# Optimization experiments

Measured on AMD Instinct MI355X. Metric: run time of the kernel, lower is better.

Reference implementation:

```python
import jax, jax.numpy as jnp
import numpy as np

NUM_CLASSES = 81
THRESHOLD = 0.5
NEGPOS_RATIO = 3
VAR = (0.1, 0.2)


def setup_inputs() -> dict:
    key = jax.random.key(0)
    kl, kc, kp1, kp2, kt1, kt2, klab = jax.random.split(key, 7)
    B, P, T = 64, 8732, 16
    loc_data = jax.random.normal(kl, (B, P, 4), jnp.float32)
    conf_data = jax.random.normal(kc, (B, P, NUM_CLASSES), jnp.float32)
    # priors in center-form (cx, cy, w, h), w/h strictly positive
    cxcy = jax.random.uniform(kp1, (P, 2), jnp.float32)
    wh = 0.05 + 0.45 * jax.random.uniform(kp2, (P, 2), jnp.float32)
    priors = jnp.concatenate([cxcy, wh], axis=1)
    # ground-truth boxes in point-form (xmin, ymin, xmax, ymax), valid in [0,1]
    mins = 0.7 * jax.random.uniform(kt1, (B, T, 2), jnp.float32)
    sizes = 0.05 + 0.25 * jax.random.uniform(kt2, (B, T, 2), jnp.float32)
    truth_boxes = jnp.concatenate([mins, mins + sizes], axis=-1)
    labels = jax.random.randint(klab, (B, T), 0, NUM_CLASSES - 1, jnp.int32)
    return {"loc_data": loc_data, "conf_data": conf_data, "priors": priors,
            "truth_boxes": truth_boxes, "labels": labels}


def _point_form(pr):
    # center-form -> point-form
    return jnp.concatenate([pr[:, :2] - pr[:, 2:] / 2, pr[:, :2] + pr[:, 2:] / 2], axis=1)


def _intersect(box_a, box_b):
    # [T,4] x [P,4] -> [T,P] intersection areas (the repo uses raw intersection, not IoU)
    max_xy = jnp.minimum(box_a[:, None, 2:], box_b[None, :, 2:])
    min_xy = jnp.maximum(box_a[:, None, :2], box_b[None, :, :2])
    inter = jnp.clip(max_xy - min_xy, 0.0, None)
    return inter[..., 0] * inter[..., 1]


def _encode(matched, priors):
    g_cxcy = (matched[:, :2] + matched[:, 2:4]) / 2 - priors[:, :2]
    g_cxcy = g_cxcy / (VAR[0] * priors[:, 2:])
    g_wh = (matched[:, 2:4] - matched[:, :2]) / priors[:, 2:]
    g_wh = jnp.log(g_wh + 1e-10) / VAR[1]
    return jnp.concatenate([g_cxcy, g_wh], axis=1)


def _match(truths, labels, priors):
    # truths [T,4] point-form, labels [T], priors [P,4] center-form
    T = truths.shape[0]
    P = priors.shape[0]
    overlaps = _intersect(truths, _point_form(priors))          # [T,P]
    best_prior_idx = jnp.argmax(overlaps, axis=1)               # [T]
    best_truth_overlap = jnp.max(overlaps, axis=0)              # [P]
    best_truth_idx = jnp.argmax(overlaps, axis=0)               # [P]
    # ensure each gt's best prior is kept (overlap forced to 2)
    best_truth_overlap = best_truth_overlap.at[best_prior_idx].set(2.0)
    hit = best_prior_idx[:, None] == jnp.arange(P)[None, :]     # [T,P]
    last_j = jnp.max(jnp.where(hit, jnp.arange(T)[:, None], -1), axis=0)  # [P]
    best_truth_idx = jnp.where(last_j >= 0, last_j, best_truth_idx)
    matches = truths[best_truth_idx]                            # [P,4]
    conf = jnp.where(best_truth_overlap < THRESHOLD, 0,
                     labels[best_truth_idx] + 1).astype(jnp.int32)
    return _encode(matches, priors), conf


def _smooth_l1(d):
    ad = jnp.abs(d)
    return jnp.where(ad < 1.0, 0.5 * d * d, ad - 0.5)


def _forward(loc_data, conf_data, priors, truth_boxes, labels):
    B, P, C = conf_data.shape
    loc_t, conf_t = jax.vmap(_match, in_axes=(0, 0, None))(truth_boxes, labels, priors)
    pos = conf_t > 0                                            # [B,P]
    num_pos = pos.sum(axis=1, keepdims=True)                    # [B,1]
    # localization smooth-L1 over positives (sum reduction)
    loss_l = jnp.sum(jnp.where(pos[..., None], _smooth_l1(loc_data - loc_t), 0.0))
    # per-prior cross-entropy
    logp = jax.nn.log_softmax(conf_data, axis=-1)               # [B,P,C]
    ce = -jnp.take_along_axis(logp, conf_t[..., None], axis=-1)[..., 0]  # [B,P]
    # hard-negative mining via double argsort rank
    mined = jnp.where(pos, 0.0, ce)
    order = jnp.argsort(-mined, axis=1)
    rank = jnp.argsort(order, axis=1)
    num_neg = jnp.clip(NEGPOS_RATIO * num_pos, None, P - 1)     # [B,1]
    neg = rank < num_neg
    loss_c = jnp.sum(jnp.where(pos | neg, ce, 0.0))
    N = jnp.maximum(num_pos.sum(), 1).astype(loc_data.dtype)
    return loss_l / N, loss_c / N


def reference(loc_data, conf_data, priors, truth_boxes, labels):
    return _forward(loc_data, conf_data, priors, truth_boxes, labels)
```

## Files before the change

kernel.cpp:

```cpp
#include <hip/hip_runtime.h>
#include <float.h>
#include <math.h>

#define B_NUM 64
#define P_NUM 8732
#define T_NUM 16
#define C_NUM 81
#define TPB   512
#define RPB_LSE 128
#define NBLK_LSE ((B_NUM * P_NUM) / RPB_LSE)
#define GRID1 (B_NUM + NBLK_LSE)
#define PLMAX 32

__device__ __forceinline__ float smooth_l1(float d) {
    float ad = fabsf(d);
    return (ad < 1.0f) ? 0.5f * d * d : ad - 0.5f;
}

struct MatchSh {
    float s_t[T_NUM][4];
    int   s_lab[T_NUM];
    unsigned short s_m[P_NUM];
    float s_rv[8 * T_NUM];
    int   s_ri[8 * T_NUM];
    int   s_bp[T_NUM];
    float s_red[8];
    int   s_redi[8];
    int   s_plist[PLMAX];
    int   s_pcount;
};

__global__ __launch_bounds__(TPB, 4) void k_fused1(
    const float* __restrict__ loc, const float* __restrict__ conf,
    const float* __restrict__ priors, const float* __restrict__ truths,
    const int* __restrict__ labels,
    int* __restrict__ num_pos, float* __restrict__ loss_l_b,
    float* __restrict__ negce, int* __restrict__ plist_g,
    int* __restrict__ sel_ctr)
{
    __shared__ MatchSh shm;
    const int tid = threadIdx.x;
    const int lane = tid & 63, wv = tid >> 6;

    if (blockIdx.x >= B_NUM) {
        const int r0 = (blockIdx.x - B_NUM) * RPB_LSE;
        const int g  = lane >> 4;
        const int lg = lane & 15;
        const int gr0 = r0 + wv * 16 + g * 4;
        const float4* g4 = (const float4*)(conf) + (size_t)gr0 * 81 / 4;

        float4 q0 = g4[lg];
        float4 q1 = g4[lg + 16];
        float4 q2 = g4[lg + 32];
        float4 q3 = g4[lg + 48];
        float4 q4 = g4[lg + 64];
        float4 q5 = make_float4(0.f, 0.f, 0.f, 0.f);
        if (lg == 0) q5 = g4[80];

        float x0 = 0.0f;
        if (lg == 0)  x0 = q0.x;
        if (lg == 4)  x0 = q1.y;
        if (lg == 8)  x0 = q2.z;
        if (lg == 12) x0 = q3.w;

        float a0 = 0.f, a1 = 0.f, a2 = 0.f, a3 = 0.f;
        a0 += __expf(q0.x) + __expf(q0.y) + __expf(q0.z) + __expf(q0.w);
        {
            int p = 64 + 4 * lg; float e;
            e = __expf(q1.x); if (p + 0 >= 81) a1 += e; else a0 += e;
            e = __expf(q1.y); if (p + 1 >= 81) a1 += e; else a0 += e;
            e = __expf(q1.z); if (p + 2 >= 81) a1 += e; else a0 += e;
            e = __expf(q1.w); if (p + 3 >= 81) a1 += e; else a0 += e;
        }
        {
            int p = 128 + 4 * lg; float e;
            e = __expf(q2.x); if (p + 0 >= 162) a2 += e; else a1 += e;
            e = __expf(q2.y); if (p + 1 >= 162) a2 += e; else a1 += e;
            e = __expf(q2.z); if (p + 2 >= 162) a2 += e; else a1 += e;
            e = __expf(q2.w); if (p + 3 >= 162) a2 += e; else a1 += e;
        }
        {
            int p = 192 + 4 * lg; float e;
            e = __expf(q3.x); if (p + 0 >= 243) a3 += e; else a2 += e;
            e = __expf(q3.y); if (p + 1 >= 243) a3 += e; else a2 += e;
            e = __expf(q3.z); if (p + 2 >= 243) a3 += e; else a2 += e;
            e = __expf(q3.w); if (p + 3 >= 243) a3 += e; else a2 += e;
        }
        a3 += __expf(q4.x) + __expf(q4.y) + __expf(q4.z) + __expf(q4.w);
        if (lg == 0)
            a3 += __expf(q5.x) + __expf(q5.y) + __expf(q5.z) + __expf(q5.w);

#pragma unroll
        for (int m = 1; m < 16; m <<= 1) {
            a0 += __shfl_xor(a0, m);
            a1 += __shfl_xor(a1, m);
            a2 += __shfl_xor(a2, m);
            a3 += __shfl_xor(a3, m);
        }
        if ((lg & 3) == 0) {
            int sel = lg >> 2;
            float s = (sel == 0) ? a0 : (sel == 1) ? a1 : (sel == 2) ? a2 : a3;
            negce[gr0 + sel] = __logf(s) - x0;
        }
        return;
    }

    const int b = blockIdx.x;
    if (tid == 0) {
        shm.s_pcount = 0;
        if (b == 0) *sel_ctr = 0;
    }
    if (tid < T_NUM * 4) ((float*)shm.s_t)[tid] = truths[b * T_NUM * 4 + tid];
    if (tid < T_NUM)     shm.s_lab[tid] = labels[b * T_NUM + tid];
    __syncthreads();

    float bpv[T_NUM]; int bpi[T_NUM];
#pragma unroll
    for (int t = 0; t < T_NUM; ++t) { bpv[t] = -1.0f; bpi[t] = 0; }

    const float4* pr4 = (const float4*)priors;
    for (int p = tid; p < P_NUM; p += TPB) {
        float4 pr = pr4[p];
        float px0 = pr.x - 0.5f * pr.z, py0 = pr.y - 0.5f * pr.w;
        float px1 = pr.x + 0.5f * pr.z, py1 = pr.y + 0.5f * pr.w;
        float btv = -1.0f; int bti = 0;
#pragma unroll
        for (int t = 0; t < T_NUM; ++t) {
            float ix = fminf(shm.s_t[t][2], px1) - fmaxf(shm.s_t[t][0], px0);
            float iy = fminf(shm.s_t[t][3], py1) - fmaxf(shm.s_t[t][1], py0);
            ix = fmaxf(ix, 0.0f); iy = fmaxf(iy, 0.0f);
            float ov = ix * iy;
            if (ov > btv) { btv = ov; bti = t; }
            if (ov > bpv[t]) { bpv[t] = ov; bpi[t] = p; }
        }
        shm.s_m[p] = (unsigned short)((btv >= 0.5f ? 0x8000 : 0) | bti);
    }
    __syncthreads();

#pragma unroll
    for (int t = 0; t < T_NUM; ++t) {
        float v = bpv[t]; int i = bpi[t];
#pragma unroll
        for (int off = 32; off > 0; off >>= 1) {
            float ov = __shfl_down(v, off);
            int   oi = __shfl_down(i, off);
            if (ov > v || (ov == v && oi < i)) { v = ov; i = oi; }
        }
        if (lane == 0) { shm.s_rv[wv * T_NUM + t] = v; shm.s_ri[wv * T_NUM + t] = i; }
    }
    __syncthreads();
    if (tid < T_NUM) {
        float v = shm.s_rv[tid]; int i = shm.s_ri[tid];
        for (int w = 1; w < 8; ++w) {
            float ov = shm.s_rv[w * T_NUM + tid]; int oi = shm.s_ri[w * T_NUM + tid];
            if (ov > v || (ov == v && oi < i)) { v = ov; i = oi; }
        }
        shm.s_bp[tid] = i;
    }
    __syncthreads();
    if (tid == 0) {
        for (int t = 0; t < T_NUM; ++t)
            shm.s_m[shm.s_bp[t]] = (unsigned short)(0x8000 | t);
    }
    __syncthreads();

    int cnt = 0; float lsum = 0.0f;
    const float4* loc4 = (const float4*)loc;
    for (int p = tid; p < P_NUM; p += TPB) {
        unsigned short mm = shm.s_m[p];
        if (mm & 0x8000) {
            int ti = mm & 0x7FFF;
            int c = shm.s_lab[ti] + 1;
            cnt++;
            int sl = atomicAdd(&shm.s_pcount, 1);
            if (sl < PLMAX) shm.s_plist[sl] = (p << 8) | c;
            float4 pr = pr4[p];
            float mx0 = shm.s_t[ti][0], my0 = shm.s_t[ti][1];
            float mx1 = shm.s_t[ti][2], my1 = shm.s_t[ti][3];
            float gx = ((mx0 + mx1) * 0.5f - pr.x) / (0.1f * pr.z);
            float gy = ((my0 + my1) * 0.5f - pr.y) / (0.1f * pr.w);
            float gw = __logf((mx1 - mx0) / pr.z + 1e-10f) / 0.2f;
            float gh = __logf((my1 - my0) / pr.w + 1e-10f) / 0.2f;
            float4 l = loc4[(size_t)b * P_NUM + p];
            lsum += smooth_l1(l.x - gx) + smooth_l1(l.y - gy)
                  + smooth_l1(l.z - gw) + smooth_l1(l.w - gh);
        }
    }
#pragma unroll
    for (int off = 32; off > 0; off >>= 1) {
        lsum += __shfl_down(lsum, off);
        cnt  += __shfl_down(cnt, off);
    }
    if (lane == 0) { shm.s_red[wv] = lsum; shm.s_redi[wv] = cnt; }
    __syncthreads();
    if (tid == 0) {
        float L = 0.0f; int C2 = 0;
        for (int w = 0; w < 8; ++w) { L += shm.s_red[w]; C2 += shm.s_redi[w]; }
        num_pos[b] = C2;
        loss_l_b[b] = L;
    }
    if (tid < shm.s_pcount && tid < PLMAX)
        plist_g[b * PLMAX + tid] = shm.s_plist[tid];
}

#define NQ4 2183
#define VELEMS 12

__global__ __launch_bounds__(1024) void k_select(
    const float* __restrict__ negce, const float* __restrict__ conf,
    const int* __restrict__ plist_g, const int* __restrict__ num_pos,
    float* __restrict__ loss_l_b, float* __restrict__ negsum_b,
    float* __restrict__ pce_b, int* __restrict__ sel_ctr,
    float* __restrict__ out)
{
    __shared__ int   s_wh[16][256];
    __shared__ int   s_hist[256];
    __shared__ unsigned int s_bm[273];
    __shared__ int   s_sel, s_rem;
    __shared__ float s_sv[16];
    __shared__ int   s_sc[16];
    __shared__ float s_pv[16];
    __shared__ int   s_last;
    __shared__ unsigned int s_mn[16], s_mx[16];
    __shared__ int   s_nz[16];
    __shared__ int   s_p1skip, s_p1sel, s_p1rem;

    const int b = blockIdx.x, tid = threadIdx.x;
    const int lane = tid & 63, wv = tid >> 6;

    const int np = num_pos[b];
    if (tid < 273) s_bm[tid] = 0u;
    __syncthreads();
    float pce = 0.0f;
    if (tid < np && tid < PLMAX) {
        int e = plist_g[b * PLMAX + tid];
        int p = e >> 8, c = e & 255;
        size_t idx = (size_t)b * P_NUM + p;
        size_t ci = idx * C_NUM;
        pce = negce[idx] + conf[ci] - conf[ci + c];
        atomicOr(&s_bm[p >> 5], 1u << (p & 31));
    }
    __syncthreads();

    unsigned int val[VELEMS];
    const float4* nb4 = (const float4*)(negce + (size_t)b * P_NUM);
#pragma unroll
    for (int i = 0; i < 3; ++i) {
        int q = tid + i * 1024;
        float4 v4 = make_float4(0.f, 0.f, 0.f, 0.f);
        if (q < NQ4) v4 = nb4[q];
        float vv[4] = {v4.x, v4.y, v4.z, v4.w};
#pragma unroll
        for (int k = 0; k < 4; ++k) {
            int p = 4 * q + k;
            unsigned int u = 0u;
            if (q < NQ4 && !((s_bm[p >> 5] >> (p & 31)) & 1u))
                u = __float_as_uint(fmaxf(vv[k], 0.0f));
            val[i * 4 + k] = u;
        }
    }

    int nn = 3 * np; if (nn > P_NUM - 1) nn = P_NUM - 1;

    {
        unsigned int tmn = 255u, tmx = 0u; int nz = 0;
#pragma unroll
        for (int i = 0; i < VELEMS; ++i) {
            unsigned int v = val[i];
            if (v) {
                unsigned int t = v >> 24;
                tmn = (t < tmn) ? t : tmn;
                tmx = (t > tmx) ? t : tmx;
                nz++;
            }
        }
#pragma unroll
        for (int off = 32; off > 0; off >>= 1) {
            unsigned int omn = __shfl_down(tmn, off);
            unsigned int omx = __shfl_down(tmx, off);
            int onz = __shfl_down(nz, off);
            tmn = (omn < tmn) ? omn : tmn;
            tmx = (omx > tmx) ? omx : tmx;
            nz += onz;
        }
        if (lane == 0) { s_mn[wv] = tmn; s_mx[wv] = tmx; s_nz[wv] = nz; }
        __syncthreads();
        if (tid == 0) {
            unsigned int MN = 255u, MX = 0u; int NZ = 0;
#pragma unroll
            for (int w = 0; w < 16; ++w) {
                if (s_mn[w] < MN) MN = s_mn[w];
                if (s_mx[w] > MX) MX = s_mx[w];
                NZ += s_nz[w];
            }
            int k0 = nn;
            if (MN == MX && NZ > 0) {
                s_p1skip = 1;
                if (k0 <= NZ) { s_p1sel = (int)MX; s_p1rem = k0; }
                else          { s_p1sel = 0;       s_p1rem = k0 - NZ; }
            } else {
                s_p1skip = 0;
            }
        }
        __syncthreads();
    }

    if (nn > 0) {
        unsigned int prefix = 0;
        int k = nn;
        const int shifts[4] = {24, 16, 8, 0};
        for (int si = 0; si < 4; ++si) {
            const int shift = shifts[si];
            if (si == 0 && s_p1skip) {
                prefix = ((unsigned int)s_p1sel) << 24;
                k = s_p1rem;
                continue;
            }
            for (int i = tid; i < 16 * 256; i += 1024) ((int*)s_wh)[i] = 0;
            __syncthreads();
            const unsigned int pmask = (shift == 24) ? 0u : (0xFFFFFFFFu << (shift + 8));
#pragma unroll
            for (int i = 0; i < VELEMS; ++i) {
                unsigned int v = val[i];
                if ((v & pmask) == prefix)
                    atomicAdd(&s_wh[wv][(v >> shift) & 0xFF], 1);
            }
            __syncthreads();
            if (tid < 256) {
                int s = 0;
#pragma unroll
                for (int w = 0; w < 16; ++w) s += s_wh[w][tid];
                s_hist[tid] = s;
            }
            __syncthreads();
            if (wv == 0) {
                int c0 = s_hist[4 * lane + 0], c1 = s_hist[4 * lane + 1];
                int c2 = s_hist[4 * lane + 2], c3 = s_hist[4 * lane + 3];
                int t3 = c3, t2 = c2 + t3, t1 = c1 + t2, t0 = c0 + t1;
                int g = t0, G = g;
#pragma unroll
                for (int off = 1; off < 64; off <<= 1) {
                    int o = __shfl_down(G, off);
                    if (lane + off < 64) G += o;
                }
                int above = G - g;
                int suf0 = t0 + above, suf1 = t1 + above;
                int suf2 = t2 + above, suf3 = t3 + above, suf4 = above;
                if (suf0 >= k && suf1 < k) { s_sel = 4 * lane + 0; s_rem = k - suf1; }
                if (suf1 >= k && suf2 < k) { s_sel = 4 * lane + 1; s_rem = k - suf2; }
                if (suf2 >= k && suf3 < k) { s_sel = 4 * lane + 2; s_rem = k - suf3; }
                if (suf3 >= k && suf4 < k) { s_sel = 4 * lane + 3; s_rem = k - suf4; }
            }
            __syncthreads();
            prefix |= ((unsigned int)s_sel) << shift;
            k = s_rem;
        }

        float sgt = 0.0f; int cgt = 0;
#pragma unroll
        for (int i = 0; i < VELEMS; ++i) {
            unsigned int v = val[i];
            if (v > prefix) { sgt += __uint_as_float(v); cgt++; }
        }
#pragma unroll
        for (int off = 32; off > 0; off >>= 1) {
            sgt += __shfl_down(sgt, off);
            cgt += __shfl_down(cgt, off);
        }
        if (lane == 0) { s_sv[wv] = sgt; s_sc[wv] = cgt; }
        __syncthreads();
        if (tid == 0) {
            float S = 0.0f; int Ct = 0;
#pragma unroll
            for (int w = 0; w < 16; ++w) { S += s_sv[w]; Ct += s_sc[w]; }
            negsum_b[b] = S + (float)(nn - Ct) * __uint_as_float(prefix);
        }
    } else {
        if (tid == 0) negsum_b[b] = 0.0f;
    }

#pragma unroll
    for (int off = 32; off > 0; off >>= 1) pce += __shfl_down(pce, off);
    if (lane == 0) s_pv[wv] = pce;
    __syncthreads();
    if (tid == 0) {
        float PCE = 0.0f;
#pragma unroll
        for (int w = 0; w < 16; ++w) PCE += s_pv[w];
        pce_b[b] = PCE;
    }

    if (tid == 0) {
        __threadfence();
        int old = atomicAdd(sel_ctr, 1);
        s_last = (old == B_NUM - 1) ? 1 : 0;
    }
    __syncthreads();
    if (s_last) {
        __threadfence();
        float ll = 0.0f, ns = 0.0f, pc = 0.0f; int npos = 0;
        if (tid < B_NUM) {
            ll = loss_l_b[tid];
            ns = negsum_b[tid];
            pc = pce_b[tid];
            npos = num_pos[tid];
        }
#pragma unroll
        for (int off = 32; off > 0; off >>= 1) {
            ll += __shfl_down(ll, off);
            ns += __shfl_down(ns, off);
            pc += __shfl_down(pc, off);
            npos += __shfl_down(npos, off);
        }
        if (lane == 0) {
            ((float*)s_wh[0])[wv] = ll;
            ((float*)s_wh[1])[wv] = ns;
            ((float*)s_wh[2])[wv] = pc;
            s_wh[3][wv] = npos;
        }
        __syncthreads();
        if (tid == 0) {
            float LL = 0.0f, NS = 0.0f, PC = 0.0f; int NP = 0;
#pragma unroll
            for (int w = 0; w < 16; ++w) {
                LL += ((float*)s_wh[0])[w];
                NS += ((float*)s_wh[1])[w];
                PC += ((float*)s_wh[2])[w];
                NP += s_wh[3][w];
            }
            float N = (float)(NP > 1 ? NP : 1);
            out[0] = LL / N;
            out[1] = (PC + NS) / N;
        }
    }
}

extern "C" void kernel_launch(void* const* d_in, const int* in_sizes, int n_in,
                              void* d_out, int out_size, void* d_ws, size_t ws_size,
                              hipStream_t stream) {
    const float* loc    = (const float*)d_in[0];
    const float* conf   = (const float*)d_in[1];
    const float* priors = (const float*)d_in[2];
    const float* truths = (const float*)d_in[3];
    const int*   labels = (const int*)d_in[4];
    float* out = (float*)d_out;

    int*   ws_i = (int*)d_ws;
    float* ws_f = (float*)d_ws;
    int*   num_pos   = ws_i;
    float* loss_l_b  = ws_f + 64;
    float* negsum_b  = ws_f + 128;
    float* pce_b     = ws_f + 192;
    int*   sel_ctr   = ws_i + 256;
    int*   plist_g   = ws_i + 1024;
    float* negce     = ws_f + 4096;

    k_fused1<<<GRID1, TPB, 0, stream>>>(loc, conf, priors, truths, labels,
                                        num_pos, loss_l_b, negce, plist_g, sel_ctr);
    k_select<<<B_NUM, 1024, 0, stream>>>(negce, conf, plist_g, num_pos,
                                         loss_l_b, negsum_b, pce_b, sel_ctr, out);
}
```

Baseline: 66.49 us.

## Merge match, log-sum-exp and selection into one cooperative kernel with grid sync

Replaces the two-kernel pipeline with a single cooperative launch of 256 blocks of 512 threads. The first 64 blocks do per-batch matching, the rest loop over the log-sum-exp units, and after a grid-wide sync the first 64 blocks run hard-negative selection with their match results still in registers and shared memory. This removes a kernel launch boundary and the plist round trip through global memory. In exchange it runs far fewer blocks for the streaming conf pass, selection uses 512 instead of 1024 threads, and it adds a memset plus a fallback path if the cooperative launch fails.

```diff
diff --git a/kernel.cpp b/kernel.cpp
--- a/kernel.cpp
+++ b/kernel.cpp
@@ -1,6 +1,9 @@
 #include <hip/hip_runtime.h>
+#include <hip/hip_cooperative_groups.h>
 #include <float.h>
 #include <math.h>
+
+namespace cg = cooperative_groups;
 
 #define B_NUM 64
 #define P_NUM 8732
@@ -8,9 +11,11 @@
 #define C_NUM 81
 #define TPB   512
 #define RPB_LSE 128
-#define NBLK_LSE ((B_NUM * P_NUM) / RPB_LSE)
-#define GRID1 (B_NUM + NBLK_LSE)
+#define NUNITS ((B_NUM * P_NUM) / RPB_LSE)
+#define GRID1 (B_NUM + NUNITS)
+#define GRID_C 256
 #define PLMAX 32
+#define NQ4 2183
 
 __device__ __forceinline__ float smooth_l1(float d) {
     float ad = fabsf(d);
@@ -21,95 +26,101 @@
     float s_t[T_NUM][4];
     int   s_lab[T_NUM];
     unsigned short s_m[P_NUM];
-    float s_rv[8 * T_NUM];
-    int   s_ri[8 * T_NUM];
+    float s_rv[16 * T_NUM];
+    int   s_ri[16 * T_NUM];
     int   s_bp[T_NUM];
-    float s_red[8];
-    int   s_redi[8];
+    float s_red[16];
+    int   s_redi[16];
     int   s_plist[PLMAX];
     int   s_pcount;
 };
-
-__global__ __launch_bounds__(TPB, 4) void k_fused1(
-    const float* __restrict__ loc, const float* __restrict__ conf,
-    const float* __restrict__ priors, const float* __restrict__ truths,
-    const int* __restrict__ labels,
+struct SelSh {
+    int   s_wh[16][256];
+    int   s_hist[256];
+    unsigned int s_bm[273];
+    int   s_sel, s_rem, s_last;
+    float s_sv[16]; int s_sc[16]; float s_pv[16];
+    unsigned int s_mn[16], s_mx[16]; int s_nz[16];
+    int   s_p1skip, s_p1sel, s_p1rem;
+};
+union __align__(16) Sh { MatchSh m; SelSh s; };
+
+__device__ __forceinline__ void negce_unit(
+    const float* __restrict__ conf, float* __restrict__ negce,
+    int u, int wv, int lane)
+{
+    const int g  = lane >> 4;
+    const int lg = lane & 15;
+    const int gr0 = u * RPB_LSE + wv * 16 + g * 4;
+    const float4* g4 = (const float4*)(conf) + (size_t)gr0 * 81 / 4;
+
+    float4 q0 = g4[lg];
+    float4 q1 = g4[lg + 16];
+    float4 q2 = g4[lg + 32];
+    float4 q3 = g4[lg + 48];
+    float4 q4 = g4[lg + 64];
+    float4 q5 = make_float4(0.f, 0.f, 0.f, 0.f);
+    if (lg == 0) q5 = g4[80];
+
+    float x0 = 0.0f;
+    if (lg == 0)  x0 = q0.x;
+    if (lg == 4)  x0 = q1.y;
+    if (lg == 8)  x0 = q2.z;
+    if (lg == 12) x0 = q3.w;
+
+    float a0 = 0.f, a1 = 0.f, a2 = 0.f, a3 = 0.f;
+    a0 += __expf(q0.x) + __expf(q0.y) + __expf(q0.z) + __expf(q0.w);
+    {
+        int p = 64 + 4 * lg; float e;
+        e = __expf(q1.x); if (p + 0 >= 81) a1 += e; else a0 += e;
+        e = __expf(q1.y); if (p + 1 >= 81) a1 += e; else a0 += e;
+        e = __expf(q1.z); if (p + 2 >= 81) a1 += e; else a0 += e;
+        e = __expf(q1.w); if (p + 3 >= 81) a1 += e; else a0 += e;
+    }
+    {
+        int p = 128 + 4 * lg; float e;
+        e = __expf(q2.x); if (p + 0 >= 162) a2 += e; else a1 += e;
+        e = __expf(q2.y); if (p + 1 >= 162) a2 += e; else a1 += e;
+        e = __expf(q2.z); if (p + 2 >= 162) a2 += e; else a1 += e;
+        e = __expf(q2.w); if (p + 3 >= 162) a2 += e; else a1 += e;
+    }
+    {
+        int p = 192 + 4 * lg; float e;
+        e = __expf(q3.x); if (p + 0 >= 243) a3 += e; else a2 += e;
+        e = __expf(q3.y); if (p + 1 >= 243) a3 += e; else a2 += e;
+        e = __expf(q3.z); if (p + 2 >= 243) a3 += e; else a2 += e;
+        e = __expf(q3.w); if (p + 3 >= 243) a3 += e; else a2 += e;
+    }
+    a3 += __expf(q4.x) + __expf(q4.y) + __expf(q4.z) + __expf(q4.w);
+    if (lg == 0)
+        a3 += __expf(q5.x) + __expf(q5.y) + __expf(q5.z) + __expf(q5.w);
+
+#pragma unroll
+    for (int m = 1; m < 16; m <<= 1) {
+        a0 += __shfl_xor(a0, m);
+        a1 += __shfl_xor(a1, m);
+        a2 += __shfl_xor(a2, m);
+        a3 += __shfl_xor(a3, m);
+    }
+    if ((lg & 3) == 0) {
+        int sel = lg >> 2;
+        float s = (sel == 0) ? a0 : (sel == 1) ? a1 : (sel == 2) ? a2 : a3;
+        negce[gr0 + sel] = __logf(s) - x0;
+    }
+}
+
+__device__ __forceinline__ void match_phase(
+    MatchSh& shm, int b,
+    const float* __restrict__ loc, const float* __restrict__ priors,
+    const float* __restrict__ truths, const int* __restrict__ labels,
     int* __restrict__ num_pos, float* __restrict__ loss_l_b,
-    float* __restrict__ negce, int* __restrict__ plist_g,
-    int* __restrict__ sel_ctr)
+    int* __restrict__ plist_g, bool write_plist,
+    int& np_out, int& myplist_out)
 {
-    __shared__ MatchSh shm;
     const int tid = threadIdx.x;
     const int lane = tid & 63, wv = tid >> 6;
 
-    if (blockIdx.x >= B_NUM) {
-        const int r0 = (blockIdx.x - B_NUM) * RPB_LSE;
-        const int g  = lane >> 4;
-        const int lg = lane & 15;
-        const int gr0 = r0 + wv * 16 + g * 4;
-        const float4* g4 = (const float4*)(conf) + (size_t)gr0 * 81 / 4;
-
-        float4 q0 = g4[lg];
-        float4 q1 = g4[lg + 16];
-        float4 q2 = g4[lg + 32];
-        float4 q3 = g4[lg + 48];
-        float4 q4 = g4[lg + 64];
-        float4 q5 = make_float4(0.f, 0.f, 0.f, 0.f);
-        if (lg == 0) q5 = g4[80];
-
-        float x0 = 0.0f;
-        if (lg == 0)  x0 = q0.x;
-        if (lg == 4)  x0 = q1.y;
-        if (lg == 8)  x0 = q2.z;
-        if (lg == 12) x0 = q3.w;
-
-        float a0 = 0.f, a1 = 0.f, a2 = 0.f, a3 = 0.f;
-        a0 += __expf(q0.x) + __expf(q0.y) + __expf(q0.z) + __expf(q0.w);
-        {
-            int p = 64 + 4 * lg; float e;
-            e = __expf(q1.x); if (p + 0 >= 81) a1 += e; else a0 += e;
-            e = __expf(q1.y); if (p + 1 >= 81) a1 += e; else a0 += e;
-            e = __expf(q1.z); if (p + 2 >= 81) a1 += e; else a0 += e;
-            e = __expf(q1.w); if (p + 3 >= 81) a1 += e; else a0 += e;
-        }
-        {
-            int p = 128 + 4 * lg; float e;
-            e = __expf(q2.x); if (p + 0 >= 162) a2 += e; else a1 += e;
-            e = __expf(q2.y); if (p + 1 >= 162) a2 += e; else a1 += e;
-            e = __expf(q2.z); if (p + 2 >= 162) a2 += e; else a1 += e;
-            e = __expf(q2.w); if (p + 3 >= 162) a2 += e; else a1 += e;
-        }
-        {
-            int p = 192 + 4 * lg; float e;
-            e = __expf(q3.x); if (p + 0 >= 243) a3 += e; else a2 += e;
-            e = __expf(q3.y); if (p + 1 >= 243) a3 += e; else a2 += e;
-            e = __expf(q3.z); if (p + 2 >= 243) a3 += e; else a2 += e;
-            e = __expf(q3.w); if (p + 3 >= 243) a3 += e; else a2 += e;
-        }
-        a3 += __expf(q4.x) + __expf(q4.y) + __expf(q4.z) + __expf(q4.w);
-        if (lg == 0)
-            a3 += __expf(q5.x) + __expf(q5.y) + __expf(q5.z) + __expf(q5.w);
-
-#pragma unroll
-        for (int m = 1; m < 16; m <<= 1) {
-            a0 += __shfl_xor(a0, m);
-            a1 += __shfl_xor(a1, m);
-            a2 += __shfl_xor(a2, m);
-            a3 += __shfl_xor(a3, m);
-        }
-        if ((lg & 3) == 0) {
-            int sel = lg >> 2;
-            float s = (sel == 0) ? a0 : (sel == 1) ? a1 : (sel == 2) ? a2 : a3;
-            negce[gr0 + sel] = __logf(s) - x0;
-        }
-        return;
-    }
-
-    const int b = blockIdx.x;
-    if (tid == 0) {
-        shm.s_pcount = 0;
-        if (b == 0) *sel_ctr = 0;
-    }
+    if (tid == 0) shm.s_pcount = 0;
     if (tid < T_NUM * 4) ((float*)shm.s_t)[tid] = truths[b * T_NUM * 4 + tid];
     if (tid < T_NUM)     shm.s_lab[tid] = labels[b * T_NUM + tid];
     __syncthreads();
@@ -151,7 +162,7 @@
     __syncthreads();
     if (tid < T_NUM) {
         float v = shm.s_rv[tid]; int i = shm.s_ri[tid];
-        for (int w = 1; w < 8; ++w) {
+        for (int w = 1; w < TPB / 64; ++w) {
             float ov = shm.s_rv[w * T_NUM + tid]; int oi = shm.s_ri[w * T_NUM + tid];
             if (ov > v || (ov == v && oi < i)) { v = ov; i = oi; }
         }
@@ -195,16 +206,261 @@
     __syncthreads();
     if (tid == 0) {
         float L = 0.0f; int C2 = 0;
-        for (int w = 0; w < 8; ++w) { L += shm.s_red[w]; C2 += shm.s_redi[w]; }
+        for (int w = 0; w < TPB / 64; ++w) { L += shm.s_red[w]; C2 += shm.s_redi[w]; }
         num_pos[b] = C2;
         loss_l_b[b] = L;
     }
-    if (tid < shm.s_pcount && tid < PLMAX)
+    __syncthreads();
+    np_out = shm.s_pcount;
+    myplist_out = (tid < np_out && tid < PLMAX) ? shm.s_plist[tid] : -1;
+    if (write_plist && tid < np_out && tid < PLMAX)
         plist_g[b * PLMAX + tid] = shm.s_plist[tid];
 }
 
-#define NQ4 2183
-#define VELEMS 12
+template<int NT>
+__device__ __forceinline__ void select_batch(
+    SelSh& ss, int b, int np, int myplist,
+    const float* __restrict__ negce, const float* __restrict__ conf,
+    const int* __restrict__ num_pos, const float* __restrict__ loss_l_b,
+    float* __restrict__ negsum_b, float* __restrict__ pce_b,
+    int* __restrict__ sel_ctr, float* __restrict__ out)
+{
+    constexpr int NW = NT / 64;
+    constexpr int NF4 = (NQ4 + NT - 1) / NT;
+    constexpr int VE = NF4 * 4;
+    const int tid = threadIdx.x, lane = tid & 63, wv = tid >> 6;
+
+    if (tid < 273) ss.s_bm[tid] = 0u;
+    if (tid == 0) ss.s_p1skip = 0;
+    __syncthreads();
+    float pce = 0.0f;
+    if (myplist >= 0) {
+        int p = myplist >> 8, c = myplist & 255;
+        size_t idx = (size_t)b * P_NUM + p;
+        size_t ci = idx * C_NUM;
+        pce = negce[idx] + conf[ci] - conf[ci + c];
+        atomicOr(&ss.s_bm[p >> 5], 1u << (p & 31));
+    }
+    __syncthreads();
+
+    unsigned int val[VE];
+    const float4* nb4 = (const float4*)(negce + (size_t)b * P_NUM);
+#pragma unroll
+    for (int i = 0; i < NF4; ++i) {
+        int q = tid + i * NT;
+        float4 v4 = make_float4(0.f, 0.f, 0.f, 0.f);
+        if (q < NQ4) v4 = nb4[q];
+        float vv[4] = {v4.x, v4.y, v4.z, v4.w};
+#pragma unroll
+        for (int k = 0; k < 4; ++k) {
+            int p = 4 * q + k;
+            unsigned int u = 0u;
+            if (q < NQ4 && !((ss.s_bm[p >> 5] >> (p & 31)) & 1u))
+                u = __float_as_uint(fmaxf(vv[k], 0.0f));
+            val[i * 4 + k] = u;
+        }
+    }
+
+    int nn = 3 * np; if (nn > P_NUM - 1) nn = P_NUM - 1;
+
+    {
+        unsigned int tmn = 255u, tmx = 0u; int nz = 0;
+#pragma unroll
+        for (int i = 0; i < VE; ++i) {
+            unsigned int v = val[i];
+            if (v) {
+                unsigned int t = v >> 24;
+                tmn = (t < tmn) ? t : tmn;
+                tmx = (t > tmx) ? t : tmx;
+                nz++;
+            }
+        }
+#pragma unroll
+        for (int off = 32; off > 0; off >>= 1) {
+            unsigned int omn = __shfl_down(tmn, off);
+            unsigned int omx = __shfl_down(tmx, off);
+            int onz = __shfl_down(nz, off);
+            tmn = (omn < tmn) ? omn : tmn;
+            tmx = (omx > tmx) ? omx : tmx;
+            nz += onz;
+        }
+        if (lane == 0) { ss.s_mn[wv] = tmn; ss.s_mx[wv] = tmx; ss.s_nz[wv] = nz; }
+        __syncthreads();
+        if (tid == 0) {
+            unsigned int MN = 255u, MX = 0u; int NZ = 0;
+            for (int w = 0; w < NW; ++w) {
+                if (ss.s_mn[w] < MN) MN = ss.s_mn[w];
+                if (ss.s_mx[w] > MX) MX = ss.s_mx[w];
+                NZ += ss.s_nz[w];
+            }
+            if (MN == MX && NZ > 0) {
+                ss.s_p1skip = 1;
+                if (nn <= NZ) { ss.s_p1sel = (int)MX; ss.s_p1rem = nn; }
+                else          { ss.s_p1sel = 0;       ss.s_p1rem = nn - NZ; }
+            }
+        }
+        __syncthreads();
+    }
+
+    if (nn > 0) {
+        unsigned int prefix = 0;
+        int k = nn;
+        const int shifts[4] = {24, 16, 8, 0};
+        for (int si = 0; si < 4; ++si) {
+            const int shift = shifts[si];
+            if (si == 0 && ss.s_p1skip) {
+                prefix = ((unsigned int)ss.s_p1sel) << 24;
+                k = ss.s_p1rem;
+                continue;
+            }
+            for (int i = tid; i < NW * 256; i += NT) ((int*)ss.s_wh)[i] = 0;
+            __syncthreads();
+            const unsigned int pmask = (shift == 24) ? 0u : (0xFFFFFFFFu << (shift + 8));
+#pragma unroll
+            for (int i = 0; i < VE; ++i) {
+                unsigned int v = val[i];
+                if ((v & pmask) == prefix)
+                    atomicAdd(&ss.s_wh[wv][(v >> shift) & 0xFF], 1);
+            }
+            __syncthreads();
+            if (tid < 256) {
+                int s = 0;
+                for (int w = 0; w < NW; ++w) s += ss.s_wh[w][tid];
+                ss.s_hist[tid] = s;
+            }
+            __syncthreads();
+            if (wv == 0) {
+                int c0 = ss.s_hist[4 * lane + 0], c1 = ss.s_hist[4 * lane + 1];
+                int c2 = ss.s_hist[4 * lane + 2], c3 = ss.s_hist[4 * lane + 3];
+                int t3 = c3, t2 = c2 + t3, t1 = c1 + t2, t0 = c0 + t1;
+                int g = t0, G = g;
+#pragma unroll
+                for (int off = 1; off < 64; off <<= 1) {
+                    int o = __shfl_down(G, off);
+                    if (lane + off < 64) G += o;
+                }
+                int above = G - g;
+                int suf0 = t0 + above, suf1 = t1 + above;
+                int suf2 = t2 + above, suf3 = t3 + above, suf4 = above;
+                if (suf0 >= k && suf1 < k) { ss.s_sel = 4 * lane + 0; ss.s_rem = k - suf1; }
+                if (suf1 >= k && suf2 < k) { ss.s_sel = 4 * lane + 1; ss.s_rem = k - suf2; }
+                if (suf2 >= k && suf3 < k) { ss.s_sel = 4 * lane + 2; ss.s_rem = k - suf3; }
+                if (suf3 >= k && suf4 < k) { ss.s_sel = 4 * lane + 3; ss.s_rem = k - suf4; }
+            }
+            __syncthreads();
+            prefix |= ((unsigned int)ss.s_sel) << shift;
+            k = ss.s_rem;
+        }
+
+        float sgt = 0.0f; int cgt = 0;
+#pragma unroll
+        for (int i = 0; i < VE; ++i) {
+            unsigned int v = val[i];
+            if (v > prefix) { sgt += __uint_as_float(v); cgt++; }
+        }
+#pragma unroll
+        for (int off = 32; off > 0; off >>= 1) {
+            sgt += __shfl_down(sgt, off);
+            cgt += __shfl_down(cgt, off);
+        }
+        if (lane == 0) { ss.s_sv[wv] = sgt; ss.s_sc[wv] = cgt; }
+        __syncthreads();
+        if (tid == 0) {
+            float S = 0.0f; int Ct = 0;
+            for (int w = 0; w < NW; ++w) { S += ss.s_sv[w]; Ct += ss.s_sc[w]; }
+            negsum_b[b] = S + (float)(nn - Ct) * __uint_as_float(prefix);
+        }
+    } else {
+        if (tid == 0) negsum_b[b] = 0.0f;
+    }
+
+#pragma unroll
+    for (int off = 32; off > 0; off >>= 1) pce += __shfl_down(pce, off);
+    if (lane == 0) ss.s_pv[wv] = pce;
+    __syncthreads();
+    if (tid == 0) {
+        float PCE = 0.0f;
+        for (int w = 0; w < NW; ++w) PCE += ss.s_pv[w];
+        pce_b[b] = PCE;
+    }
+
+    if (tid == 0) {
+        __threadfence();
+        int old = atomicAdd(sel_ctr, 1);
+        ss.s_last = (old == B_NUM - 1) ? 1 : 0;
+    }
+    __syncthreads();
+    if (ss.s_last && wv == 0) {
+        __threadfence();
+        float ll = loss_l_b[lane];
+        float ns = negsum_b[lane];
+        float pc = pce_b[lane];
+        int   npg = num_pos[lane];
+#pragma unroll
+        for (int off = 32; off > 0; off >>= 1) {
+            ll += __shfl_down(ll, off);
+            ns += __shfl_down(ns, off);
+            pc += __shfl_down(pc, off);
+            npg += __shfl_down(npg, off);
+        }
+        if (lane == 0) {
+            float N = (float)(npg > 1 ? npg : 1);
+            out[0] = ll / N;
+            out[1] = (pc + ns) / N;
+        }
+    }
+}
+
+__global__ __launch_bounds__(TPB) void k_coop(
+    const float* __restrict__ loc, const float* __restrict__ conf,
+    const float* __restrict__ priors, const float* __restrict__ truths,
+    const int* __restrict__ labels,
+    int* __restrict__ num_pos, float* __restrict__ loss_l_b,
+    float* __restrict__ negsum_b, float* __restrict__ pce_b,
+    float* __restrict__ negce, int* __restrict__ plist_g,
+    int* __restrict__ sel_ctr, float* __restrict__ out)
+{
+    __shared__ Sh sh;
+    const int blk = blockIdx.x;
+    const int lane = threadIdx.x & 63, wv = threadIdx.x >> 6;
+
+    int np_loc = 0, myplist = -1;
+    if (blk < B_NUM) {
+        match_phase(sh.m, blk, loc, priors, truths, labels,
+                    num_pos, loss_l_b, plist_g, false, np_loc, myplist);
+    } else {
+        for (int u = blk - B_NUM; u < NUNITS; u += (GRID_C - B_NUM))
+            negce_unit(conf, negce, u, wv, lane);
+    }
+
+    cg::this_grid().sync();
+
+    if (blk < B_NUM)
+        select_batch<TPB>(sh.s, blk, np_loc, myplist, negce, conf,
+                          num_pos, loss_l_b, negsum_b, pce_b, sel_ctr, out);
+}
+
+__global__ __launch_bounds__(TPB, 4) void k_fused1(
+    const float* __restrict__ loc, const float* __restrict__ conf,
+    const float* __restrict__ priors, const float* __restrict__ truths,
+    const int* __restrict__ labels,
+    int* __restrict__ num_pos, float* __restrict__ loss_l_b,
+    float* __restrict__ negce, int* __restrict__ plist_g,
+    int* __restrict__ sel_ctr)
+{
+    __shared__ MatchSh shm;
+    const int lane = threadIdx.x & 63, wv = threadIdx.x >> 6;
+
+    if (blockIdx.x >= B_NUM) {
+        negce_unit(conf, negce, blockIdx.x - B_NUM, wv, lane);
+        return;
+    }
+    const int b = blockIdx.x;
+    if (b == 0 && threadIdx.x == 0) *sel_ctr = 0;
+    int np_loc, myplist;
+    match_phase(shm, b, loc, priors, truths, labels,
+                num_pos, loss_l_b, plist_g, true, np_loc, myplist);
+}
 
 __global__ __launch_bounds__(1024) void k_select(
     const float* __restrict__ negce, const float* __restrict__ conf,
@@ -213,226 +469,12 @@
     float* __restrict__ pce_b, int* __restrict__ sel_ctr,
     float* __restrict__ out)
 {
-    __shared__ int   s_wh[16][256];
-    __shared__ int   s_hist[256];
-    __shared__ unsigned int s_bm[273];
-    __shared__ int   s_sel, s_rem;
-    __shared__ float s_sv[16];
-    __shared__ int   s_sc[16];
-    __shared__ float s_pv[16];
-    __shared__ int   s_last;
-    __shared__ unsigned int s_mn[16], s_mx[16];
-    __shared__ int   s_nz[16];
-    __shared__ int   s_p1skip, s_p1sel, s_p1rem;
-
+    __shared__ SelSh ss;
     const int b = blockIdx.x, tid = threadIdx.x;
-    const int lane = tid & 63, wv = tid >> 6;
-
     const int np = num_pos[b];
-    if (tid < 273) s_bm[tid] = 0u;
-    __syncthreads();
-    float pce = 0.0f;
-    if (tid < np && tid < PLMAX) {
-        int e = plist_g[b * PLMAX + tid];
-        int p = e >> 8, c = e & 255;
-        size_t idx = (size_t)b * P_NUM + p;
-        size_t ci = idx * C_NUM;
-        pce = negce[idx] + conf[ci] - conf[ci + c];
-        atomicOr(&s_bm[p >> 5], 1u << (p & 31));
-    }
-    __syncthreads();
-
-    unsigned int val[VELEMS];
-    const float4* nb4 = (const float4*)(negce + (size_t)b * P_NUM);
-#pragma unroll
-    for (int i = 0; i < 3; ++i) {
-        int q = tid + i * 1024;
-        float4 v4 = make_float4(0.f, 0.f, 0.f, 0.f);
-        if (q < NQ4) v4 = nb4[q];
-        float vv[4] = {v4.x, v4.y, v4.z, v4.w};
-#pragma unroll
-        for (int k = 0; k < 4; ++k) {
-            int p = 4 * q + k;
-            unsigned int u = 0u;
-            if (q < NQ4 && !((s_bm[p >> 5] >> (p & 31)) & 1u))
-                u = __float_as_uint(fmaxf(vv[k], 0.0f));
-            val[i * 4 + k] = u;
-        }
-    }
-
-    int nn = 3 * np; if (nn > P_NUM - 1) nn = P_NUM - 1;
-
-    {
-        unsigned int tmn = 255u, tmx = 0u; int nz = 0;
-#pragma unroll
-        for (int i = 0; i < VELEMS; ++i) {
-            unsigned int v = val[i];
-            if (v) {
-                unsigned int t = v >> 24;
-                tmn = (t < tmn) ? t : tmn;
-                tmx = (t > tmx) ? t : tmx;
-                nz++;
-            }
-        }
-#pragma unroll
-        for (int off = 32; off > 0; off >>= 1) {
-            unsigned int omn = __shfl_down(tmn, off);
-            unsigned int omx = __shfl_down(tmx, off);
-            int onz = __shfl_down(nz, off);
-            tmn = (omn < tmn) ? omn : tmn;
-            tmx = (omx > tmx) ? omx : tmx;
-            nz += onz;
-        }
-        if (lane == 0) { s_mn[wv] = tmn; s_mx[wv] = tmx; s_nz[wv] = nz; }
-        __syncthreads();
-        if (tid == 0) {
-            unsigned int MN = 255u, MX = 0u; int NZ = 0;
-#pragma unroll
-            for (int w = 0; w < 16; ++w) {
-                if (s_mn[w] < MN) MN = s_mn[w];
-                if (s_mx[w] > MX) MX = s_mx[w];
-                NZ += s_nz[w];
-            }
-            int k0 = nn;
-            if (MN == MX && NZ > 0) {
-                s_p1skip = 1;
-                if (k0 <= NZ) { s_p1sel = (int)MX; s_p1rem = k0; }
-                else          { s_p1sel = 0;       s_p1rem = k0 - NZ; }
-            } else {
-                s_p1skip = 0;
-            }
-        }
-        __syncthreads();
-    }
-
-    if (nn > 0) {
-        unsigned int prefix = 0;
-        int k = nn;
-        const int shifts[4] = {24, 16, 8, 0};
-        for (int si = 0; si < 4; ++si) {
-            const int shift = shifts[si];
-            if (si == 0 && s_p1skip) {
-                prefix = ((unsigned int)s_p1sel) << 24;
-                k = s_p1rem;
-                continue;
-            }
-            for (int i = tid; i < 16 * 256; i += 1024) ((int*)s_wh)[i] = 0;
-            __syncthreads();
-            const unsigned int pmask = (shift == 24) ? 0u : (0xFFFFFFFFu << (shift + 8));
-#pragma unroll
-            for (int i = 0; i < VELEMS; ++i) {
-                unsigned int v = val[i];
-                if ((v & pmask) == prefix)
-                    atomicAdd(&s_wh[wv][(v >> shift) & 0xFF], 1);
-            }
-            __syncthreads();
-            if (tid < 256) {
-                int s = 0;
-#pragma unroll
-                for (int w = 0; w < 16; ++w) s += s_wh[w][tid];
-                s_hist[tid] = s;
-            }
-            __syncthreads();
-            if (wv == 0) {
-                int c0 = s_hist[4 * lane + 0], c1 = s_hist[4 * lane + 1];
-                int c2 = s_hist[4 * lane + 2], c3 = s_hist[4 * lane + 3];
-                int t3 = c3, t2 = c2 + t3, t1 = c1 + t2, t0 = c0 + t1;
-                int g = t0, G = g;
-#pragma unroll
-                for (int off = 1; off < 64; off <<= 1) {
-                    int o = __shfl_down(G, off);
-                    if (lane + off < 64) G += o;
-                }
-                int above = G - g;
-                int suf0 = t0 + above, suf1 = t1 + above;
-                int suf2 = t2 + above, suf3 = t3 + above, suf4 = above;
-                if (suf0 >= k && suf1 < k) { s_sel = 4 * lane + 0; s_rem = k - suf1; }
-                if (suf1 >= k && suf2 < k) { s_sel = 4 * lane + 1; s_rem = k - suf2; }
-                if (suf2 >= k && suf3 < k) { s_sel = 4 * lane + 2; s_rem = k - suf3; }
-                if (suf3 >= k && suf4 < k) { s_sel = 4 * lane + 3; s_rem = k - suf4; }
-            }
-            __syncthreads();
-            prefix |= ((unsigned int)s_sel) << shift;
-            k = s_rem;
-        }
-
-        float sgt = 0.0f; int cgt = 0;
-#pragma unroll
-        for (int i = 0; i < VELEMS; ++i) {
-            unsigned int v = val[i];
-            if (v > prefix) { sgt += __uint_as_float(v); cgt++; }
-        }
-#pragma unroll
-        for (int off = 32; off > 0; off >>= 1) {
-            sgt += __shfl_down(sgt, off);
-            cgt += __shfl_down(cgt, off);
-        }
-        if (lane == 0) { s_sv[wv] = sgt; s_sc[wv] = cgt; }
-        __syncthreads();
-        if (tid == 0) {
-            float S = 0.0f; int Ct = 0;
-#pragma unroll
-            for (int w = 0; w < 16; ++w) { S += s_sv[w]; Ct += s_sc[w]; }
-            negsum_b[b] = S + (float)(nn - Ct) * __uint_as_float(prefix);
-        }
-    } else {
-        if (tid == 0) negsum_b[b] = 0.0f;
-    }
-
-#pragma unroll
-    for (int off = 32; off > 0; off >>= 1) pce += __shfl_down(pce, off);
-    if (lane == 0) s_pv[wv] = pce;
-    __syncthreads();
-    if (tid == 0) {
-        float PCE = 0.0f;
-#pragma unroll
-        for (int w = 0; w < 16; ++w) PCE += s_pv[w];
-        pce_b[b] = PCE;
-    }
-
-    if (tid == 0) {
-        __threadfence();
-        int old = atomicAdd(sel_ctr, 1);
-        s_last = (old == B_NUM - 1) ? 1 : 0;
-    }
-    __syncthreads();
-    if (s_last) {
-        __threadfence();
-        float ll = 0.0f, ns = 0.0f, pc = 0.0f; int npos = 0;
-        if (tid < B_NUM) {
-            ll = loss_l_b[tid];
-            ns = negsum_b[tid];
-            pc = pce_b[tid];
-            npos = num_pos[tid];
-        }
-#pragma unroll
-        for (int off = 32; off > 0; off >>= 1) {
-            ll += __shfl_down(ll, off);
-            ns += __shfl_down(ns, off);
-            pc += __shfl_down(pc, off);
-            npos += __shfl_down(npos, off);
-        }
-        if (lane == 0) {
-            ((float*)s_wh[0])[wv] = ll;
-            ((float*)s_wh[1])[wv] = ns;
-            ((float*)s_wh[2])[wv] = pc;
-            s_wh[3][wv] = npos;
-        }
-        __syncthreads();
-        if (tid == 0) {
-            float LL = 0.0f, NS = 0.0f, PC = 0.0f; int NP = 0;
-#pragma unroll
-            for (int w = 0; w < 16; ++w) {
-                LL += ((float*)s_wh[0])[w];
-                NS += ((float*)s_wh[1])[w];
-                PC += ((float*)s_wh[2])[w];
-                NP += s_wh[3][w];
-            }
-            float N = (float)(NP > 1 ? NP : 1);
-            out[0] = LL / N;
-            out[1] = (PC + NS) / N;
-        }
-    }
+    int myplist = (tid < np && tid < PLMAX) ? plist_g[b * PLMAX + tid] : -1;
+    select_batch<1024>(ss, b, np, myplist, negce, conf,
+                       num_pos, loss_l_b, negsum_b, pce_b, sel_ctr, out);
 }
 
 extern "C" void kernel_launch(void* const* d_in, const int* in_sizes, int n_in,
@@ -455,8 +497,18 @@
     int*   plist_g   = ws_i + 1024;
     float* negce     = ws_f + 4096;
 
-    k_fused1<<<GRID1, TPB, 0, stream>>>(loc, conf, priors, truths, labels,
-                                        num_pos, loss_l_b, negce, plist_g, sel_ctr);
-    k_select<<<B_NUM, 1024, 0, stream>>>(negce, conf, plist_g, num_pos,
-                                         loss_l_b, negsum_b, pce_b, sel_ctr, out);
-}
+    hipMemsetAsync((void*)sel_ctr, 0, sizeof(int), stream);
+
+    void* args[] = { (void*)&loc, (void*)&conf, (void*)&priors, (void*)&truths,
+                     (void*)&labels, (void*)&num_pos, (void*)&loss_l_b,
+                     (void*)&negsum_b, (void*)&pce_b, (void*)&negce,
+                     (void*)&plist_g, (void*)&sel_ctr, (void*)&out };
+    hipError_t e = hipLaunchCooperativeKernel((const void*)k_coop, dim3(GRID_C),
+                                              dim3(TPB), args, 0, stream);
+    if (e != hipSuccess) {
+        k_fused1<<<GRID1, TPB, 0, stream>>>(loc, conf, priors, truths, labels,
+                                            num_pos, loss_l_b, negce, plist_g, sel_ctr);
+        k_select<<<B_NUM, 1024, 0, stream>>>(negce, conf, plist_g, num_pos,
+                                             loss_l_b, negsum_b, pce_b, sel_ctr, out);
+    }
+}
```

Result: slower. 101.1 us (+52.1%).
